# Kernel optimization log

Measured on AMD Instinct MI355X. Metric: run time of the kernel, lower is better.

## Reference

```python
import jax, jax.numpy as jnp
import numpy as np

SEQ = 2048
HID = 1024
NH = 16
HD = HID // NH


def setup_inputs() -> dict:
    key = jax.random.key(0)
    ks = jax.random.split(key, 5)
    s = 0.02
    return {
        "hidden_states": jax.random.normal(ks[0], (SEQ, HID), dtype=jnp.float32),
        "w_attn": jax.random.normal(ks[1], (HID, 3 * HID), dtype=jnp.float32) * s,
        "b_attn": jax.random.normal(ks[2], (3 * HID,), dtype=jnp.float32) * s,
        "w_proj": jax.random.normal(ks[3], (HID, HID), dtype=jnp.float32) * s,
        "b_proj": jax.random.normal(ks[4], (HID,), dtype=jnp.float32) * s,
    }


def reference(hidden_states, w_attn, b_attn, w_proj, b_proj):
    S = hidden_states.shape[0]
    qkv = hidden_states @ w_attn + b_attn          # [S, 3H]
    q, k, v = jnp.split(qkv, 3, axis=-1)
    q = q.reshape(S, NH, HD)
    k = k.reshape(S, NH, HD)
    v = v.reshape(S, NH, HD)
    sm_scale = 1.0 / np.sqrt(HD).astype(np.float32)
    # explicit scores [h, q, k] in fp32, as in the torch module
    scores = jnp.einsum('qhd,khd->hqk', q.astype(jnp.float32), k.astype(jnp.float32))
    scores = scores * sm_scale
    causal = jnp.tril(jnp.ones((S, S), dtype=bool))  # [q, k]
    scores = jnp.where(causal[None, :, :], scores, -jnp.inf)
    probs = jax.nn.softmax(scores, axis=-1)
    attn = jnp.einsum('hqk,khd->qhd', probs, v.astype(jnp.float32))  # [S, NH, HD]
    attn = attn.reshape(S, HID).astype(hidden_states.dtype)
    return attn @ w_proj + b_proj
```

## Files before the change

### kernel.cpp

```cpp
#include <hip/hip_runtime.h>
#include <cstdint>
#include <cstddef>

#define SEQ 2048
#define HID 1024
#define NHEAD 16
#define HDIM 64

typedef _Float16 f16;
typedef f16 half8 __attribute__((ext_vector_type(8)));
typedef f16 half4 __attribute__((ext_vector_type(4)));
typedef f16 half2_ __attribute__((ext_vector_type(2)));
typedef float f32x4 __attribute__((ext_vector_type(4)));

#define ASYNC_COPY16(g, l)                                                    \
  __builtin_amdgcn_global_load_lds(                                           \
      (const __attribute__((address_space(1))) void*)(const void*)(g),        \
      (__attribute__((address_space(3))) void*)(void*)(l), 16, 0, 0)

__global__ __launch_bounds__(256) void prologue(
    const float* __restrict__ h, const float* __restrict__ wa,
    const float* __restrict__ wp, f16* __restrict__ h16,
    f16* __restrict__ waT, f16* __restrict__ wpT) {
  const int b = blockIdx.x, tid = threadIdx.x;
  if (b >= 4096) {
    int i = ((b - 4096) * 256 + tid) * 4;
    float4 v = *(const float4*)(h + i);
    half4 o;
    o[0] = (f16)v.x; o[1] = (f16)v.y; o[2] = (f16)v.z; o[3] = (f16)v.w;
    *(half4*)(h16 + i) = o;
    return;
  }
  const float* src; f16* dst; int C, bx, by;
  if (b < 3072) { src = wa; dst = waT; C = 3072; bx = b % 96; by = b / 96; }
  else { int t = b - 3072; src = wp; dst = wpT; C = 1024; bx = t & 31; by = t >> 5; }
  __shared__ float tile[32][33];
  const int tx = tid & 31, ty = tid >> 5;
  const int c0 = bx * 32, r0 = by * 32;
#pragma unroll
  for (int i = 0; i < 32; i += 8)
    tile[ty + i][tx] = src[(size_t)(r0 + ty + i) * C + c0 + tx];
  __syncthreads();
#pragma unroll
  for (int i = 0; i < 32; i += 8)
    dst[(size_t)(c0 + ty + i) * 1024 + r0 + tx] = (f16)tile[tx][ty + i];
}

template <int BM, int BN, bool OUT16>
__global__ __launch_bounds__(256) void gemm_f16(
    const f16* __restrict__ A, const f16* __restrict__ Bt,
    const float* __restrict__ bias, void* __restrict__ Cout, int M, int N,
    int K) {
  constexpr int FM = BM / 32, FN = BN / 32;
  __shared__ __align__(16) f16 sA[BM * 32];
  __shared__ __align__(16) f16 sB[BN * 32];
  const int tid = threadIdx.x;
  const int wave = tid >> 6, lane = tid & 63;
  const int quad = lane >> 4, l16 = lane & 15;
  const int m0 = blockIdx.y * BM, n0 = blockIdx.x * BN;
  const int wm = (wave >> 1) * (BM / 2), wn = (wave & 1) * (BN / 2);
  const int rowA = lane >> 2, chunkA = lane & 3;

  f32x4 acc[FM][FN] = {};

  for (int k0 = 0; k0 < K; k0 += 32) {
#pragma unroll
    for (int r = wave; r < BM / 16; r += 4)
      ASYNC_COPY16(A + (size_t)(m0 + r * 16 + rowA) * K + k0 + chunkA * 8,
                   &sA[r * 512]);
#pragma unroll
    for (int r = wave; r < BN / 16; r += 4)
      ASYNC_COPY16(Bt + (size_t)(n0 + r * 16 + rowA) * K + k0 + chunkA * 8,
                   &sB[r * 512]);
    __syncthreads();

    half8 af[FM], bf[FN];
#pragma unroll
    for (int i = 0; i < FM; i++)
      af[i] = *(const half8*)&sA[(wm + i * 16 + l16) * 32 + quad * 8];
#pragma unroll
    for (int j = 0; j < FN; j++)
      bf[j] = *(const half8*)&sB[(wn + j * 16 + l16) * 32 + quad * 8];
#pragma unroll
    for (int i = 0; i < FM; i++)
#pragma unroll
      for (int j = 0; j < FN; j++)
        acc[i][j] = __builtin_amdgcn_mfma_f32_16x16x32_f16(af[i], bf[j],
                                                           acc[i][j], 0, 0, 0);
    __syncthreads();
  }

#pragma unroll
  for (int i = 0; i < FM; i++) {
    int row = m0 + wm + i * 16 + quad * 4;
#pragma unroll
    for (int j = 0; j < FN; j++) {
      int col = n0 + wn + j * 16 + l16;
      float bv = bias[col];
#pragma unroll
      for (int r = 0; r < 4; r++) {
        float v = acc[i][j][r] + bv;
        if (OUT16)
          ((f16*)Cout)[(size_t)(row + r) * N + col] = (f16)v;
        else
          ((float*)Cout)[(size_t)(row + r) * N + col] = v;
      }
    }
  }
}

#define LROW 72
__global__ __launch_bounds__(256, 3) void attn_split(
    const f16* __restrict__ qkv, f16* __restrict__ out,
    f16* __restrict__ Opart, float* __restrict__ ml) {
  const int b = blockIdx.x;
  const int h = b / 40;
  const int t = b % 40;
  int m, c, nc;
  if (t < 4)       { m = t;                 c = 0;      nc = 1; }
  else if (t < 12) { int u = t - 4;  m = 4 + (u >> 1);  c = u & 1; nc = 2; }
  else if (t < 24) { int u = t - 12; m = 8 + u / 3;     c = u % 3; nc = 3; }
  else             { int u = t - 24; m = 12 + (u >> 2); c = u & 3; nc = 4; }
  const int q0 = m * 128;
  const int T = 2 * m + 2;
  const int kt0 = c * 8;
  const int kt1 = (kt0 + 8 < T) ? kt0 + 8 : T;
  const int maskFrom = 2 * m;

  __shared__ __align__(16) f16 sK[64 * LROW];
  __shared__ __align__(16) f16 sVt[64 * LROW];
  __shared__ __align__(16) f16 sP[4][32 * LROW];

  const int tid = threadIdx.x;
  const int wave = tid >> 6, lane = tid & 63;
  const int quad = lane >> 4, l16 = lane & 15;

  const f16 qs = (f16)0.18033688f;
  half8 qf[2][2];
#pragma unroll
  for (int g = 0; g < 2; g++) {
    const f16* qb = qkv + (size_t)(q0 + wave * 32 + g * 16 + l16) * 3072 +
                    h * HDIM + quad * 8;
    qf[g][0] = *(const half8*)qb;
    qf[g][1] = *(const half8*)(qb + 32);
#pragma unroll
    for (int j = 0; j < 8; j++) { qf[g][0][j] *= qs; qf[g][1][j] *= qs; }
  }

  const f16* kbase = qkv + HID + h * HDIM;
  const f16* vbase = qkv + 2 * HID + h * HDIM;
  const int ks_row = tid >> 3, ks_cc = tid & 7;
  const int vs_d = tid & 63, vs_g = tid >> 6;

  f32x4 o[2][4] = {};
  float m_i[2] = {-1e30f, -1e30f}, l_i[2] = {0.f, 0.f};
  half8 kreg[2], vreg[2];

  auto prefetch = [&](int kt) {
    const int k0 = kt * 64;
#pragma unroll
    for (int i = 0; i < 2; i++) {
      kreg[i] = *(const half8*)(kbase + (size_t)(k0 + ks_row + i * 32) * 3072 +
                                ks_cc * 8);
      half8 col;
#pragma unroll
      for (int j = 0; j < 8; j++)
        col[j] = vbase[(size_t)(k0 + (vs_g + i * 4) * 8 + j) * 3072 + vs_d];
      vreg[i] = col;
    }
  };

  prefetch(kt0);
  for (int kt = kt0; kt < kt1; kt++) {
    const int k0 = kt * 64;
#pragma unroll
    for (int i = 0; i < 2; i++) {
      *(half8*)&sK[(ks_row + i * 32) * LROW + ks_cc * 8] = kreg[i];
      *(half8*)&sVt[vs_d * LROW + (vs_g + i * 4) * 8] = vreg[i];
    }
    __syncthreads();
    if (kt + 1 < kt1) prefetch(kt + 1);

    f32x4 sacc[2][4] = {};
#pragma unroll
    for (int kb = 0; kb < 4; kb++) {
      half8 kf0 = *(const half8*)&sK[(kb * 16 + l16) * LROW + quad * 8];
      half8 kf1 = *(const half8*)&sK[(kb * 16 + l16) * LROW + 32 + quad * 8];
#pragma unroll
      for (int g = 0; g < 2; g++) {
        sacc[g][kb] = __builtin_amdgcn_mfma_f32_16x16x32_f16(kf0, qf[g][0],
                                                             sacc[g][kb], 0, 0, 0);
        sacc[g][kb] = __builtin_amdgcn_mfma_f32_16x16x32_f16(kf1, qf[g][1],
                                                             sacc[g][kb], 0, 0, 0);
      }
    }
    if (kt >= maskFrom) {
#pragma unroll
      for (int g = 0; g < 2; g++) {
        const int qg = q0 + wave * 32 + g * 16 + l16;
#pragma unroll
        for (int kb = 0; kb < 4; kb++) {
          int kg = k0 + kb * 16 + quad * 4;
#pragma unroll
          for (int r = 0; r < 4; r++)
            if (kg + r > qg) sacc[g][kb][r] = -1e30f;
        }
      }
    }
#pragma unroll
    for (int g = 0; g < 2; g++) {
      float mx = -1e30f;
#pragma unroll
      for (int kb = 0; kb < 4; kb++)
#pragma unroll
        for (int r = 0; r < 4; r++) mx = fmaxf(mx, sacc[g][kb][r]);
      mx = fmaxf(mx, __shfl_xor(mx, 16));
      mx = fmaxf(mx, __shfl_xor(mx, 32));
      const float mnew = fmaxf(m_i[g], mx);
      const float alpha = exp2f(m_i[g] - mnew);
      float rs = 0.f;
#pragma unroll
      for (int kb = 0; kb < 4; kb++)
#pragma unroll
        for (int r = 0; r < 4; r++) {
          float p = exp2f(sacc[g][kb][r] - mnew);
          sacc[g][kb][r] = p;
          rs += p;
        }
      rs += __shfl_xor(rs, 16);
      rs += __shfl_xor(rs, 32);
      l_i[g] = l_i[g] * alpha + rs;
      m_i[g] = mnew;
#pragma unroll
      for (int j = 0; j < 4; j++)
#pragma unroll
        for (int r = 0; r < 4; r++) o[g][j][r] *= alpha;
      f16* pw = &sP[wave][(g * 16 + l16) * LROW];
#pragma unroll
      for (int kb = 0; kb < 4; kb++)
#pragma unroll
        for (int rp = 0; rp < 2; rp++) {
          half2_ pv;
          pv[0] = (f16)sacc[g][kb][rp * 2];
          pv[1] = (f16)sacc[g][kb][rp * 2 + 1];
          *(half2_*)&pw[kb * 16 + quad * 4 + rp * 2] = pv;
        }
    }
#pragma unroll
    for (int j = 0; j < 4; j++) {
      half8 vf0 = *(const half8*)&sVt[(j * 16 + l16) * LROW + quad * 8];
      half8 vf1 = *(const half8*)&sVt[(j * 16 + l16) * LROW + 32 + quad * 8];
#pragma unroll
      for (int g = 0; g < 2; g++) {
        half8 pf0 = *(const half8*)&sP[wave][(g * 16 + l16) * LROW + quad * 8];
        half8 pf1 =
            *(const half8*)&sP[wave][(g * 16 + l16) * LROW + 32 + quad * 8];
        o[g][j] = __builtin_amdgcn_mfma_f32_16x16x32_f16(vf0, pf0, o[g][j], 0, 0, 0);
        o[g][j] = __builtin_amdgcn_mfma_f32_16x16x32_f16(vf1, pf1, o[g][j], 0, 0, 0);
      }
    }
    __syncthreads();
  }

  if (nc == 1) {
#pragma unroll
    for (int g = 0; g < 2; g++) {
      const float inv = 1.f / l_i[g];
      f16* orow =
          out + (size_t)(q0 + wave * 32 + g * 16 + l16) * HID + h * HDIM;
#pragma unroll
      for (int j = 0; j < 4; j++) {
        half4 hv;
#pragma unroll
        for (int r = 0; r < 4; r++) hv[r] = (f16)(o[g][j][r] * inv);
        *(half4*)&orow[j * 16 + quad * 4] = hv;
      }
    }
  } else {
    int base;
    if (m < 8)       base = (m - 4) * 2;
    else if (m < 12) base = 8 + (m - 8) * 3;
    else             base = 20 + (m - 12) * 4;
    const int slot = h * 36 + base + c;
#pragma unroll
    for (int g = 0; g < 2; g++) {
      const int qrow = wave * 32 + g * 16 + l16;
      f16* op = Opart + (size_t)slot * 8192 + qrow * 64;
#pragma unroll
      for (int j = 0; j < 4; j++) {
        half4 hv;
#pragma unroll
        for (int r = 0; r < 4; r++) hv[r] = (f16)o[g][j][r];
        *(half4*)&op[j * 16 + quad * 4] = hv;
      }
      if (quad == 0) {
        ml[slot * 256 + qrow] = m_i[g];
        ml[slot * 256 + 128 + qrow] = l_i[g];
      }
    }
  }
}

__global__ __launch_bounds__(256) void attn_combine(
    const f16* __restrict__ Opart, const float* __restrict__ ml,
    f16* __restrict__ out) {
  int idx = blockIdx.x * 256 + threadIdx.x;
  int d = idx & 63;
  int row = (idx >> 6) & 127;
  int rest = idx >> 13;
  int mi = rest % 12;
  int h = rest / 12;
  int m = 4 + mi;
  int nc = (mi < 4) ? 2 : (mi < 8) ? 3 : 4;
  int base = (mi < 4) ? mi * 2 : (mi < 8) ? 8 + (mi - 4) * 3 : 20 + (mi - 8) * 4;
  int slot0 = h * 36 + base;

  float mm[4], ll[4];
  float M = -1e30f;
  for (int cc = 0; cc < nc; cc++) {
    mm[cc] = ml[(slot0 + cc) * 256 + row];
    ll[cc] = ml[(slot0 + cc) * 256 + 128 + row];
    M = fmaxf(M, mm[cc]);
  }
  float L = 0.f, acc = 0.f;
  for (int cc = 0; cc < nc; cc++) {
    float w = exp2f(mm[cc] - M);
    L += w * ll[cc];
    acc += w * (float)Opart[(size_t)(slot0 + cc) * 8192 + row * 64 + d];
  }
  out[(size_t)(m * 128 + row) * HID + h * HDIM + d] = (f16)(acc / L);
}

extern "C" void kernel_launch(void* const* d_in, const int* in_sizes, int n_in,
                              void* d_out, int out_size, void* d_ws,
                              size_t ws_size, hipStream_t stream) {
  const float* h = (const float*)d_in[0];
  const float* wa = (const float*)d_in[1];
  const float* ba = (const float*)d_in[2];
  const float* wp = (const float*)d_in[3];
  const float* bp = (const float*)d_in[4];
  float* out = (float*)d_out;

  char* ws = (char*)d_ws;
  f16* h16 = (f16*)(ws);
  f16* waT = (f16*)(ws + (4u << 20));
  f16* wpT = (f16*)(ws + (10u << 20));
  f16* qkv = (f16*)(ws + (12u << 20));
  f16* attn = (f16*)(ws + (24u << 20));
  f16* Opart = (f16*)(ws);
  float* mlbuf = (float*)(ws + 9437184);

  prologue<<<6144, 256, 0, stream>>>(h, wa, wp, h16, waT, wpT);
  gemm_f16<128, 128, true><<<dim3(24, 16), 256, 0, stream>>>(
      h16, waT, ba, qkv, SEQ, 3 * HID, HID);
  attn_split<<<640, 256, 0, stream>>>(qkv, attn, Opart, mlbuf);
  attn_combine<<<6144, 256, 0, stream>>>(Opart, mlbuf, attn);
  gemm_f16<64, 64, false><<<dim3(16, 32), 256, 0, stream>>>(
      attn, wpT, bp, out, SEQ, HID, HID);
}
```

Baseline: 161.1 us.

## Load K fragments directly from global, double-buffer V, lazy softmax rescale

```diff
diff --git a/kernel.cpp b/kernel.cpp
--- a/kernel.cpp
+++ b/kernel.cpp
@@ -113,7 +113,7 @@
 __global__ __launch_bounds__(256, 3) void attn_split(
     const f16* __restrict__ qkv, f16* __restrict__ out,
     f16* __restrict__ Opart, float* __restrict__ ml) {
-  const int b = blockIdx.x;
+  const int b = (blockIdx.x & 7) * 80 + (blockIdx.x >> 3);
   const int h = b / 40;
   const int t = b % 40;
   int m, c, nc;
@@ -127,8 +127,7 @@
   const int kt1 = (kt0 + 8 < T) ? kt0 + 8 : T;
   const int maskFrom = 2 * m;
 
-  __shared__ __align__(16) f16 sK[64 * LROW];
-  __shared__ __align__(16) f16 sVt[64 * LROW];
+  __shared__ __align__(16) f16 sVt[2][64 * LROW];
   __shared__ __align__(16) f16 sP[4][32 * LROW];
 
   const int tid = threadIdx.x;
@@ -149,19 +148,16 @@
 
   const f16* kbase = qkv + HID + h * HDIM;
   const f16* vbase = qkv + 2 * HID + h * HDIM;
-  const int ks_row = tid >> 3, ks_cc = tid & 7;
   const int vs_d = tid & 63, vs_g = tid >> 6;
 
   f32x4 o[2][4] = {};
   float m_i[2] = {-1e30f, -1e30f}, l_i[2] = {0.f, 0.f};
-  half8 kreg[2], vreg[2];
-
-  auto prefetch = [&](int kt) {
+  half8 vreg[2];
+
+  auto vprefetch = [&](int kt) {
     const int k0 = kt * 64;
 #pragma unroll
     for (int i = 0; i < 2; i++) {
-      kreg[i] = *(const half8*)(kbase + (size_t)(k0 + ks_row + i * 32) * 3072 +
-                                ks_cc * 8);
       half8 col;
 #pragma unroll
       for (int j = 0; j < 8; j++)
@@ -169,23 +165,27 @@
       vreg[i] = col;
     }
   };
-
-  prefetch(kt0);
+  auto vstore = [&](int buf) {
+#pragma unroll
+    for (int i = 0; i < 2; i++)
+      *(half8*)&sVt[buf][vs_d * LROW + (vs_g + i * 4) * 8] = vreg[i];
+  };
+
+  vprefetch(kt0);
+  vstore(0);
+  __syncthreads();
+
   for (int kt = kt0; kt < kt1; kt++) {
+    const int cur = (kt - kt0) & 1;
     const int k0 = kt * 64;
-#pragma unroll
-    for (int i = 0; i < 2; i++) {
-      *(half8*)&sK[(ks_row + i * 32) * LROW + ks_cc * 8] = kreg[i];
-      *(half8*)&sVt[vs_d * LROW + (vs_g + i * 4) * 8] = vreg[i];
-    }
-    __syncthreads();
-    if (kt + 1 < kt1) prefetch(kt + 1);
+    if (kt + 1 < kt1) vprefetch(kt + 1);
 
     f32x4 sacc[2][4] = {};
+    const f16* krow = kbase + (size_t)(k0 + l16) * 3072 + quad * 8;
 #pragma unroll
     for (int kb = 0; kb < 4; kb++) {
-      half8 kf0 = *(const half8*)&sK[(kb * 16 + l16) * LROW + quad * 8];
-      half8 kf1 = *(const half8*)&sK[(kb * 16 + l16) * LROW + 32 + quad * 8];
+      half8 kf0 = *(const half8*)(krow + (size_t)kb * 16 * 3072);
+      half8 kf1 = *(const half8*)(krow + (size_t)kb * 16 * 3072 + 32);
 #pragma unroll
       for (int g = 0; g < 2; g++) {
         sacc[g][kb] = __builtin_amdgcn_mfma_f32_16x16x32_f16(kf0, qf[g][0],
@@ -216,25 +216,28 @@
         for (int r = 0; r < 4; r++) mx = fmaxf(mx, sacc[g][kb][r]);
       mx = fmaxf(mx, __shfl_xor(mx, 16));
       mx = fmaxf(mx, __shfl_xor(mx, 32));
-      const float mnew = fmaxf(m_i[g], mx);
-      const float alpha = exp2f(m_i[g] - mnew);
+      if (!__all(mx <= m_i[g] + 8.f)) {
+        const float mnew = fmaxf(m_i[g], mx);
+        const float alpha = exp2f(m_i[g] - mnew);
+        l_i[g] *= alpha;
+#pragma unroll
+        for (int j = 0; j < 4; j++)
+#pragma unroll
+          for (int r = 0; r < 4; r++) o[g][j][r] *= alpha;
+        m_i[g] = mnew;
+      }
       float rs = 0.f;
 #pragma unroll
       for (int kb = 0; kb < 4; kb++)
 #pragma unroll
         for (int r = 0; r < 4; r++) {
-          float p = exp2f(sacc[g][kb][r] - mnew);
+          float p = exp2f(sacc[g][kb][r] - m_i[g]);
           sacc[g][kb][r] = p;
           rs += p;
         }
       rs += __shfl_xor(rs, 16);
       rs += __shfl_xor(rs, 32);
-      l_i[g] = l_i[g] * alpha + rs;
-      m_i[g] = mnew;
-#pragma unroll
-      for (int j = 0; j < 4; j++)
-#pragma unroll
-        for (int r = 0; r < 4; r++) o[g][j][r] *= alpha;
+      l_i[g] += rs;
       f16* pw = &sP[wave][(g * 16 + l16) * LROW];
 #pragma unroll
       for (int kb = 0; kb < 4; kb++)
@@ -246,19 +249,23 @@
           *(half2_*)&pw[kb * 16 + quad * 4 + rp * 2] = pv;
         }
     }
+    half8 pf[2][2];
+#pragma unroll
+    for (int g = 0; g < 2; g++) {
+      pf[g][0] = *(const half8*)&sP[wave][(g * 16 + l16) * LROW + quad * 8];
+      pf[g][1] = *(const half8*)&sP[wave][(g * 16 + l16) * LROW + 32 + quad * 8];
+    }
 #pragma unroll
     for (int j = 0; j < 4; j++) {
-      half8 vf0 = *(const half8*)&sVt[(j * 16 + l16) * LROW + quad * 8];
-      half8 vf1 = *(const half8*)&sVt[(j * 16 + l16) * LROW + 32 + quad * 8];
+      half8 vf0 = *(const half8*)&sVt[cur][(j * 16 + l16) * LROW + quad * 8];
+      half8 vf1 = *(const half8*)&sVt[cur][(j * 16 + l16) * LROW + 32 + quad * 8];
 #pragma unroll
       for (int g = 0; g < 2; g++) {
-        half8 pf0 = *(const half8*)&sP[wave][(g * 16 + l16) * LROW + quad * 8];
-        half8 pf1 =
-            *(const half8*)&sP[wave][(g * 16 + l16) * LROW + 32 + quad * 8];
-        o[g][j] = __builtin_amdgcn_mfma_f32_16x16x32_f16(vf0, pf0, o[g][j], 0, 0, 0);
-        o[g][j] = __builtin_amdgcn_mfma_f32_16x16x32_f16(vf1, pf1, o[g][j], 0, 0, 0);
-      }
-    }
+        o[g][j] = __builtin_amdgcn_mfma_f32_16x16x32_f16(vf0, pf[g][0], o[g][j], 0, 0, 0);
+        o[g][j] = __builtin_amdgcn_mfma_f32_16x16x32_f16(vf1, pf[g][1], o[g][j], 0, 0, 0);
+      }
+    }
+    if (kt + 1 < kt1) vstore(cur ^ 1);
     __syncthreads();
   }
 
```

Result: slower. 169.1 us (+5.0%).
